# Performance work log

Hardware: AMD Instinct MI355X
Metric: run time of the kernel (lower is better)

The kernel has to match this reference:

```python
import jax, jax.numpy as jnp
import numpy as np
from jax import lax

B, H0, W0 = 8, 64, 64
DIM, HEADS, WS, SR = 128, 4, 3, 8
HD = DIM // HEADS
LOCAL = WS * WS
L_TAB = 1024
HIDDEN = int(2 * int(DIM * 4.0) / 3)  # ConvolutionalGLU hidden = 341


def _ln(x, g, b):
    m = jnp.mean(x, -1, keepdims=True)
    v = jnp.mean((x - m) ** 2, -1, keepdims=True)
    return (x - m) * lax.rsqrt(v + 1e-5) * g + b


def _l2(x):
    n = jnp.sqrt(jnp.sum(x * x, -1, keepdims=True))
    return x / jnp.maximum(n, 1e-12)


def _forward(x, norm1_g, norm1_b, q_w, kv_w, temperature, query_embedding,
             rel_bias_local, learnable_tokens, learnable_bias, sr_w, sr_b,
             normp_g, normp_b, cpb1_w, cpb1_b, cpb2_w, cpb2_b, proj_w, proj_b,
             norm2_g, norm2_b, fc1_w, fc1_b, dw_w, dw_b, fc2_w, fc2_b,
             relative_coords_table, seq_length_scale,
             relative_pos_index, padding_mask, H, W):
    Bn, N, C = x.shape
    pH, pW = H // SR, W // SR
    PL = pH * pW
    h = _ln(x, norm1_g, norm1_b)
    # ---- AggregatedAttention ----
    q = (h @ q_w.T).reshape(Bn, N, HEADS, HD).transpose(0, 2, 1, 3)  # bhnd
    q_norm = _l2(q)
    q_s = (q_norm + query_embedding) * jax.nn.softplus(temperature) * seq_length_scale
    kv = h @ kv_w.T  # (B, N, 2C)
    k_loc = _l2(kv[..., :C].reshape(Bn, N, HEADS, HD)).reshape(Bn, N, C)
    kv_loc = jnp.concatenate([k_loc, kv[..., C:]], -1).transpose(0, 2, 1).reshape(Bn, 2 * C, H, W)
    p = WS // 2
    xp = jnp.pad(kv_loc, ((0, 0), (0, 0), (p, p), (p, p)))
    # nn.Unfold(ws, pad=ws//2, stride=1): channel-major patches -> (B, 2C, LOCAL, N)
    pat = jnp.stack([xp[:, :, i:i + H, j:j + W] for i in range(WS) for j in range(WS)], axis=2)
    pat = pat.reshape(Bn, 2 * HEADS, HD, LOCAL, N).transpose(0, 1, 4, 2, 3)  # b 2h n d l
    k_l, v_l = pat[:, :HEADS], pat[:, HEADS:]
    attn_local = jnp.einsum('bhnd,bhndl->bhnl', q_s, k_l) + rel_bias_local[:, None, :]
    attn_local = jnp.where(padding_mask, -jnp.inf, attn_local)
    # pooled (global) branch
    xi = h.transpose(0, 2, 1).reshape(Bn, C, H, W)
    xi = jax.nn.gelu(jnp.einsum('oc,bchw->bohw', sr_w, xi) + sr_b[None, :, None, None], approximate=False)
    xi = xi.reshape(Bn, C, pH, SR, pW, SR).mean(axis=(3, 5)).reshape(Bn, C, PL).transpose(0, 2, 1)
    xi = _ln(xi, normp_g, normp_b)
    kvp = (xi @ kv_w.T).reshape(Bn, PL, 2 * HEADS, HD).transpose(0, 2, 1, 3)
    k_p, v_p = kvp[:, :HEADS], kvp[:, HEADS:]
    # CPB MLP bias; runtime size == trained size so both bilinear interps are identity
    t = jax.nn.relu(relative_coords_table @ cpb1_w.T + cpb1_b) @ cpb2_w.T + cpb2_b  # (L, heads)
    pb = t.T[:, relative_pos_index.reshape(-1)].reshape(HEADS, N, PL)
    attn_pool = jnp.einsum('bhnd,bhpd->bhnp', q_s, _l2(k_p)) + pb[None]
    attn = jax.nn.softmax(jnp.concatenate([attn_local, attn_pool], -1), axis=-1)
    a_l, a_p = attn[..., :LOCAL], attn[..., LOCAL:]
    l_mix = jnp.einsum('bhnd,hdl->bhnl', q_norm, learnable_tokens) + learnable_bias + a_l
    x_l = jnp.einsum('bhnl,bhndl->bhnd', l_mix, v_l)
    x_p = jnp.einsum('bhnp,bhpd->bhnd', a_p, v_p)
    attn_out = (x_l + x_p).transpose(0, 2, 1, 3).reshape(Bn, N, C) @ proj_w.T + proj_b
    x = x + attn_out
    # ---- ConvolutionalGLU MLP ----
    h2 = _ln(x, norm2_g, norm2_b)
    u = h2 @ fc1_w.T + fc1_b
    g1, v1 = u[..., :HIDDEN], u[..., HIDDEN:]
    gi = g1.transpose(0, 2, 1).reshape(Bn, HIDDEN, H, W)
    gi = lax.conv_general_dilated(gi, dw_w, (1, 1), 'SAME',
                                  feature_group_count=HIDDEN,
                                  dimension_numbers=('NCHW', 'OIHW', 'NCHW')) + dw_b[None, :, None, None]
    gi = gi.reshape(Bn, HIDDEN, N).transpose(0, 2, 1)
    mlp = (jax.nn.gelu(gi, approximate=False) * v1) @ fc2_w.T + fc2_b
    return x + mlp


def setup_inputs():
    key = jax.random.key(0)
    ks = jax.random.split(key, 16)
    N = H0 * W0
    PL = (H0 // SR) * (W0 // SR)
    r = lambda i, shape, s=0.02: jax.random.normal(ks[i], shape, jnp.float32) * s
    return {
        'x': jax.random.normal(ks[0], (B, N, DIM), jnp.float32),
        'norm1_g': jnp.ones((DIM,)), 'norm1_b': jnp.zeros((DIM,)),
        'q_w': r(1, (DIM, DIM)), 'kv_w': r(2, (2 * DIM, DIM)),
        'temperature': jnp.full((HEADS, 1, 1), float(np.log(np.expm1(1.0 / 0.24))), jnp.float32),
        'query_embedding': r(3, (HEADS, 1, HD)),
        'rel_bias_local': r(4, (HEADS, LOCAL), 0.0004),
        'learnable_tokens': r(5, (HEADS, HD, LOCAL)),
        'learnable_bias': jnp.zeros((HEADS, 1, LOCAL)),
        'sr_w': r(6, (DIM, DIM)), 'sr_b': jnp.zeros((DIM,)),
        'normp_g': jnp.ones((DIM,)), 'normp_b': jnp.zeros((DIM,)),
        'cpb1_w': r(7, (512, 2)), 'cpb1_b': jnp.zeros((512,)),
        'cpb2_w': r(8, (HEADS, 512)), 'cpb2_b': jnp.zeros((HEADS,)),
        'proj_w': r(9, (DIM, DIM)), 'proj_b': jnp.zeros((DIM,)),
        'norm2_g': jnp.ones((DIM,)), 'norm2_b': jnp.zeros((DIM,)),
        'fc1_w': r(10, (2 * HIDDEN, DIM)), 'fc1_b': jnp.zeros((2 * HIDDEN,)),
        'dw_w': r(11, (HIDDEN, 1, 3, 3)), 'dw_b': jnp.zeros((HIDDEN,)),
        'fc2_w': r(12, (DIM, HIDDEN)), 'fc2_b': jnp.zeros((DIM,)),
        'relative_coords_table': jax.random.uniform(ks[13], (L_TAB, 2), jnp.float32, -1.0, 1.0),
        'seq_length_scale': jnp.array([float(np.log(N + PL))], jnp.float32),
        'relative_pos_index': jax.random.randint(ks[14], (N, PL), 0, L_TAB),
        'padding_mask': jnp.zeros((B, 1, N, LOCAL), bool),
        'H': H0, 'W': W0,
    }


def reference(x, norm1_g, norm1_b, q_w, kv_w, temperature, query_embedding,
              rel_bias_local, learnable_tokens, learnable_bias, sr_w, sr_b,
              normp_g, normp_b, cpb1_w, cpb1_b, cpb2_w, cpb2_b, proj_w, proj_b,
              norm2_g, norm2_b, fc1_w, fc1_b, dw_w, dw_b, fc2_w, fc2_b,
              relative_coords_table, seq_length_scale,
              relative_pos_index, padding_mask, H, W):
    return _forward(x, norm1_g, norm1_b, q_w, kv_w, temperature, query_embedding,
                    rel_bias_local, learnable_tokens, learnable_bias, sr_w, sr_b,
                    normp_g, normp_b, cpb1_w, cpb1_b, cpb2_w, cpb2_b, proj_w, proj_b,
                    norm2_g, norm2_b, fc1_w, fc1_b, dw_w, dw_b, fc2_w, fc2_b,
                    relative_coords_table, seq_length_scale,
                    relative_pos_index, padding_mask, H, W)
```

## Files before the change

kernel.cpp:

```cpp
#include <hip/hip_runtime.h>
#include <hip/hip_bf16.h>
#include <math.h>

#define NTOK 4096
#define CDIM 128

typedef __attribute__((ext_vector_type(4))) float f32x4;
typedef __attribute__((ext_vector_type(8))) short bfx8;

__device__ __forceinline__ float geluf(float z){
  return 0.5f*z*(1.0f+erff(z*0.70710678118654752440f));
}
__device__ __forceinline__ float softplusf(float x){
  return (x>20.0f)?x:log1pf(expf(x));
}
__device__ __forceinline__ ushort f2bf(float f){
  __hip_bfloat16 h=__float2bfloat16(f);
  return *reinterpret_cast<ushort*>(&h);
}

__global__ __launch_bounds__(256) void convw_kernel(
  const float* __restrict__ projw, const float* __restrict__ fc1w,
  const float* __restrict__ fc2w,
  ushort* __restrict__ pwb, ushort* __restrict__ f1wb, ushort* __restrict__ f2wb){
  int id=blockIdx.x*256+threadIdx.x;
  if(id<16384) pwb[id]=f2bf(projw[id]);
  else if(id<106496){ int t=id-16384; int nn=t>>7,k=t&127;
    f1wb[t]=f2bf(nn<682? fc1w[nn*128+k] : 0.0f); }
  else if(id<155648){ int t=id-106496; int nn=t/384,k=t-nn*384;
    f2wb[t]=f2bf(k<341? fc2w[nn*341+k] : 0.0f); }
}

__global__ __launch_bounds__(128) void ln_f32_kernel(const float* __restrict__ in,
    const float* __restrict__ g, const float* __restrict__ bb, float* __restrict__ out){
  int t=blockIdx.x, c=threadIdx.x;
  float v=in[(size_t)t*CDIM+c];
  __shared__ float red[2];
  float s=v;
  #pragma unroll
  for(int m=1;m<64;m<<=1) s+=__shfl_xor(s,m);
  if((c&63)==0) red[c>>6]=s;
  __syncthreads();
  float mean=(red[0]+red[1])*(1.0f/CDIM);
  float d=v-mean;
  __syncthreads();
  float s2=d*d;
  #pragma unroll
  for(int m=1;m<64;m<<=1) s2+=__shfl_xor(s2,m);
  if((c&63)==0) red[c>>6]=s2;
  __syncthreads();
  float var=(red[0]+red[1])*(1.0f/CDIM);
  out[(size_t)t*CDIM+c]=d*rsqrtf(var+1e-5f)*g[c]+bb[c];
}

__global__ __launch_bounds__(128) void ln_bf_kernel(const float* __restrict__ in,
    const float* __restrict__ g, const float* __restrict__ bb, ushort* __restrict__ out){
  int t=blockIdx.x, c=threadIdx.x;
  float v=in[(size_t)t*CDIM+c];
  __shared__ float red[2];
  float s=v;
  #pragma unroll
  for(int m=1;m<64;m<<=1) s+=__shfl_xor(s,m);
  if((c&63)==0) red[c>>6]=s;
  __syncthreads();
  float mean=(red[0]+red[1])*(1.0f/CDIM);
  float d=v-mean;
  __syncthreads();
  float s2=d*d;
  #pragma unroll
  for(int m=1;m<64;m<<=1) s2+=__shfl_xor(s2,m);
  if((c&63)==0) red[c>>6]=s2;
  __syncthreads();
  float var=(red[0]+red[1])*(1.0f/CDIM);
  out[(size_t)t*CDIM+c]=f2bf(d*rsqrtf(var+1e-5f)*g[c]+bb[c]);
}

__global__ __launch_bounds__(128) void qproj_kernel(const float* __restrict__ h,
  const float* __restrict__ qw, const float* __restrict__ qemb,
  const float* __restrict__ temp, const float* __restrict__ seqs,
  float* __restrict__ qsout, float* __restrict__ qnout){
  int t0=blockIdx.x*8;
  int o=threadIdx.x;
  __shared__ float hr[8][128];
  for(int i=o;i<1024;i+=128) hr[i>>7][i&127]=h[(size_t)t0*128+i];
  __syncthreads();
  const float* wr=qw+(size_t)o*128;
  float a[8]={0,0,0,0,0,0,0,0};
  for(int c=0;c<128;c++){
    float wv=wr[c];
    #pragma unroll
    for(int tt=0;tt<8;tt++) a[tt]+=hr[tt][c]*wv;
  }
  int hh=o>>5, d=o&31;
  float emb=qemb[hh*32+d];
  float scale=softplusf(temp[hh])*seqs[0];
  #pragma unroll
  for(int tt=0;tt<8;tt++){
    float ss=a[tt]*a[tt];
    #pragma unroll
    for(int m=1;m<32;m<<=1) ss+=__shfl_xor(ss,m);
    float qnv=a[tt]/fmaxf(sqrtf(ss),1e-12f);
    qnout[(size_t)(t0+tt)*128+o]=qnv;
    qsout[(size_t)(t0+tt)*128+o]=(qnv+emb)*scale;
  }
}

__global__ __launch_bounds__(256) void kvproj_kernel(const float* __restrict__ h,
  const float* __restrict__ kvw, float* __restrict__ kv_tm){
  int t0=blockIdx.x*8;
  int tid=threadIdx.x;
  __shared__ float hr[8][128];
  for(int i=tid;i<1024;i+=256) hr[i>>7][i&127]=h[(size_t)t0*128+i];
  __syncthreads();
  const float* wr=kvw+(size_t)tid*128;
  float a[8]={0,0,0,0,0,0,0,0};
  for(int c=0;c<128;c++){
    float wv=wr[c];
    #pragma unroll
    for(int tt=0;tt<8;tt++) a[tt]+=hr[tt][c]*wv;
  }
  #pragma unroll
  for(int tt=0;tt<8;tt++){
    float v=a[tt];
    if(tid<128){
      float ss=v*v;
      #pragma unroll
      for(int m=1;m<32;m<<=1) ss+=__shfl_xor(ss,m);
      v/=fmaxf(sqrtf(ss),1e-12f);
    }
    kv_tm[(size_t)(t0+tt)*256+tid]=v;
  }
}

__global__ __launch_bounds__(128) void srpool_kernel(const float* __restrict__ h,
  const float* __restrict__ srw, const float* __restrict__ srb, float* __restrict__ xipre){
  int bp=blockIdx.x;
  int b=bp>>6, pp=bp&63;
  int py=pp>>3, px=pp&7;
  int o=threadIdx.x;
  __shared__ float hr[64][128];
  for(int i=0;i<64;i++){
    int yy=py*8+(i>>3), xx=px*8+(i&7);
    hr[i][o]=h[((size_t)b*NTOK+yy*64+xx)*128+o];
  }
  __syncthreads();
  const float* wr=srw+(size_t)o*128;
  float bias=srb[o];
  float acc=0;
  for(int i=0;i<64;i++){
    float s=bias;
    for(int c=0;c<128;c++) s+=hr[i][c]*wr[c];
    acc+=geluf(s);
  }
  xipre[(size_t)bp*128+o]=acc*(1.0f/64.0f);
}

__global__ __launch_bounds__(256) void kvp_kernel(const float* __restrict__ xi,
  const float* __restrict__ kvw, float* __restrict__ kpb, float* __restrict__ vpb){
  int bp=blockIdx.x;
  int b=bp>>6, p=bp&63;
  int o=threadIdx.x;
  __shared__ float xr[128];
  if(o<128) xr[o]=xi[(size_t)bp*128+o];
  __syncthreads();
  const float* wr=kvw+(size_t)o*128;
  float acc=0;
  for(int c=0;c<128;c++) acc+=xr[c]*wr[c];
  int hh=(o>>5)&3, d=o&31;
  if(o<128){
    float ss=acc*acc;
    #pragma unroll
    for(int m=1;m<32;m<<=1) ss+=__shfl_xor(ss,m);
    acc/=fmaxf(sqrtf(ss),1e-12f);
    kpb[(((size_t)b*4+hh)*64+p)*32+d]=acc;
  } else {
    vpb[(((size_t)b*4+hh)*64+p)*32+d]=acc;
  }
}

__global__ __launch_bounds__(256) void cpb_kernel(const float* __restrict__ tbl,
  const float* __restrict__ w1, const float* __restrict__ b1,
  const float* __restrict__ w2, const float* __restrict__ b2, float* __restrict__ tout){
  int i=blockIdx.x;
  float c0=tbl[i*2], c1=tbl[i*2+1];
  int tid=threadIdx.x;
  float p0=0,p1=0,p2=0,p3=0;
  for(int j=tid;j<512;j+=256){
    float r=fmaxf(c0*w1[j*2]+c1*w1[j*2+1]+b1[j],0.0f);
    p0+=r*w2[j]; p1+=r*w2[512+j]; p2+=r*w2[1024+j]; p3+=r*w2[1536+j];
  }
  #pragma unroll
  for(int m=1;m<64;m<<=1){
    p0+=__shfl_xor(p0,m); p1+=__shfl_xor(p1,m);
    p2+=__shfl_xor(p2,m); p3+=__shfl_xor(p3,m);
  }
  __shared__ float red[4][4];
  int w=tid>>6;
  if((tid&63)==0){ red[w][0]=p0; red[w][1]=p1; red[w][2]=p2; red[w][3]=p3; }
  __syncthreads();
  if(tid<4)
    tout[(size_t)i*4+tid]=red[0][tid]+red[1][tid]+red[2][tid]+red[3][tid]+b2[tid];
}

__global__ __launch_bounds__(256) void attn3b_kernel(
  const float* __restrict__ qs, const float* __restrict__ qn,
  const float* __restrict__ kv_tm, const float* __restrict__ kp,
  const float* __restrict__ vp, const float* __restrict__ tb,
  const int* __restrict__ rpi, const float* __restrict__ relb,
  const float* __restrict__ ltok, const float* __restrict__ lbias,
  ushort* __restrict__ mid){
  int n0=blockIdx.x*4, h=blockIdx.y, b=blockIdx.z;
  int tt=threadIdx.x>>6, lane=threadIdx.x&63;
  int n=n0+tt;
  int y=n>>6, x=n&63;
  __shared__ float kp_s[64][33];
  __shared__ float vp_s[64][33];
  __shared__ float qs_s[4][32], qn_s[4][32];
  __shared__ float ap_sh[4][64];
  __shared__ float lm_sh[4][9];
  {
    size_t kb=((size_t)(b*4+h))*2048;
    for(int i=threadIdx.x;i<2048;i+=256){
      kp_s[i>>5][i&31]=kp[kb+i];
      vp_s[i>>5][i&31]=vp[kb+i];
    }
  }
  if(lane<32) qs_s[tt][lane]=qs[((size_t)b*NTOK+n)*128+h*32+lane];
  else        qn_s[tt][lane-32]=qn[((size_t)b*NTOK+n)*128+h*32+(lane-32)];
  __syncthreads();
  float lp;
  {
    float s=0;
    #pragma unroll
    for(int d=0;d<32;d++) s+=qs_s[tt][d]*kp_s[lane][d];
    lp=s+tb[(size_t)rpi[(size_t)n*64+lane]*4+h];
  }
  bool lval=lane<9;
  float ll=0.0f;
  if(lval){
    int dy=lane/3-1, dx=lane%3-1;
    int yy=y+dy, xx=x+dx;
    float s=0;
    if(yy>=0&&yy<64&&xx>=0&&xx<64){
      const float* kr=kv_tm+((size_t)b*NTOK+(size_t)(yy*64+xx))*256+h*32;
      #pragma unroll
      for(int d=0;d<32;d++) s+=qs_s[tt][d]*kr[d];
    }
    ll=s+relb[h*9+lane];
  }
  float m=lp; if(lval) m=fmaxf(m,ll);
  #pragma unroll
  for(int o=1;o<64;o<<=1) m=fmaxf(m,__shfl_xor(m,o));
  float ep=expf(lp-m);
  float el=lval?expf(ll-m):0.0f;
  float ssum=ep+el;
  #pragma unroll
  for(int o=1;o<64;o<<=1) ssum+=__shfl_xor(ssum,o);
  float inv=1.0f/ssum;
  ap_sh[tt][lane]=ep*inv;
  if(lval){
    float lm=lbias[h*9+lane]+el*inv;
    #pragma unroll
    for(int d=0;d<32;d++) lm+=qn_s[tt][d]*ltok[(size_t)(h*32+d)*9+lane];
    lm_sh[tt][lane]=lm;
  }
  __syncthreads();
  if(lane<32){
    int d=lane;
    float acc=0;
    #pragma unroll
    for(int l=0;l<9;l++){
      int dy=l/3-1, dx=l%3-1;
      int yy=y+dy, xx=x+dx;
      if(yy>=0&&yy<64&&xx>=0&&xx<64)
        acc+=lm_sh[tt][l]*kv_tm[((size_t)b*NTOK+(size_t)(yy*64+xx))*256+128+h*32+d];
    }
    #pragma unroll
    for(int p=0;p<64;p++) acc+=ap_sh[tt][p]*vp_s[p][d];
    mid[((size_t)b*NTOK+n)*128+h*32+d]=f2bf(acc);
  }
}

template<int KTILES,int EPI>
__global__ __launch_bounds__(256) void gemm_kernel(
  const ushort* __restrict__ A, const ushort* __restrict__ W,
  const float* __restrict__ bias, const float* __restrict__ resid,
  float* __restrict__ out, int Nreal){
  const int Kt=KTILES*128;
  int m0=blockIdx.x*128, n0=blockIdx.y*64;
  int tid=threadIdx.x;
  int wave=tid>>6, lane=tid&63;
  __shared__ ushort lA[128*128];
  __shared__ ushort lB[64*128];
  f32x4 acc[4][2]={};
  int wm=(wave>>1)*64, wn=(wave&1)*32;
  for(int kc=0;kc<KTILES;kc++){
    __syncthreads();
    #pragma unroll
    for(int it=0;it<8;it++){
      int id=it*256+tid;
      int kb=id&15, m=id>>4;
      uint4 v=*(const uint4*)(A+(size_t)(m0+m)*Kt+kc*128+kb*8);
      int byte=(m*256+kb*16)^((m&7)<<4);
      *(uint4*)((char*)lA+byte)=v;
    }
    #pragma unroll
    for(int it=0;it<4;it++){
      int id=it*256+tid;
      int kb=id&15, n=id>>4;
      uint4 v=*(const uint4*)(W+(size_t)(n0+n)*Kt+kc*128+kb*8);
      int byte=(n*256+kb*16)^((n&7)<<4);
      *(uint4*)((char*)lB+byte)=v;
    }
    __syncthreads();
    #pragma unroll
    for(int ks=0;ks<4;ks++){
      int kb=ks*4+(lane>>4);
      bfx8 bfr[2];
      #pragma unroll
      for(int nr=0;nr<2;nr++){
        int n=wn+nr*16+(lane&15);
        int byte=(n*256+kb*16)^((n&7)<<4);
        bfr[nr]=*(bfx8*)((char*)lB+byte);
      }
      #pragma unroll
      for(int mr=0;mr<4;mr++){
        int m=wm+mr*16+(lane&15);
        int byte=(m*256+kb*16)^((m&7)<<4);
        bfx8 afr=*(bfx8*)((char*)lA+byte);
        acc[mr][0]=__builtin_amdgcn_mfma_f32_16x16x32_bf16(afr,bfr[0],acc[mr][0],0,0,0);
        acc[mr][1]=__builtin_amdgcn_mfma_f32_16x16x32_bf16(afr,bfr[1],acc[mr][1],0,0,0);
      }
    }
  }
  int g=lane>>4, li=lane&15;
  #pragma unroll
  for(int mr=0;mr<4;mr++){
    #pragma unroll
    for(int r=0;r<4;r++){
      int row=m0+wm+mr*16+g*4+r;
      #pragma unroll
      for(int nr=0;nr<2;nr++){
        int col=n0+wn+nr*16+li;
        float v=acc[mr][nr][r];
        if constexpr(EPI==0){
          if(col<Nreal) out[(size_t)row*682+col]=v+bias[col];
        } else {
          out[(size_t)row*128+col]=v+bias[col]+resid[(size_t)row*128+col];
        }
      }
    }
  }
}

__global__ __launch_bounds__(256) void dwconv_kernel(const float* __restrict__ u,
    const float* __restrict__ dww, const float* __restrict__ dwb, ushort* __restrict__ act){
  int c0=blockIdx.x*32;
  int cwReal=341-c0; if(cwReal>32) cwReal=32;
  int y0=blockIdx.y*2;
  int b=blockIdx.z;
  int tid=threadIdx.x;
  __shared__ float gsh[4][64][33];
  for(int it=0;it<32;it++){
    int idx=it*256+tid;
    int cc=idx&31;
    int px=(idx>>5)&63;
    int row=idx>>11;
    int yy=y0-1+row;
    float v=0.0f;
    if(yy>=0&&yy<64&&cc<cwReal)
      v=u[((size_t)b*NTOK+yy*64+px)*682+c0+cc];
    gsh[row][px][cc]=v;
  }
  __syncthreads();
  int cc=tid&31, pxb=tid>>5;
  int c=c0+cc;
  if(c>=384) return;
  if(cc<cwReal){
    float w0=dww[c*9+0],w1=dww[c*9+1],w2=dww[c*9+2],
          w3=dww[c*9+3],w4=dww[c*9+4],w5=dww[c*9+5],
          w6=dww[c*9+6],w7=dww[c*9+7],w8=dww[c*9+8];
    float bias=dwb[c];
    for(int ty=0;ty<2;ty++){
      for(int pxi=0;pxi<8;pxi++){
        int px=pxi*8+pxb;
        float ss=0.0f;
        if(px>0){ ss+=gsh[ty][px-1][cc]*w0+gsh[ty+1][px-1][cc]*w3+gsh[ty+2][px-1][cc]*w6; }
        ss+=gsh[ty][px][cc]*w1+gsh[ty+1][px][cc]*w4+gsh[ty+2][px][cc]*w7;
        if(px<63){ ss+=gsh[ty][px+1][cc]*w2+gsh[ty+1][px+1][cc]*w5+gsh[ty+2][px+1][cc]*w8; }
        float z=ss+bias;
        int nn=(y0+ty)*64+px;
        float gate=u[((size_t)b*NTOK+nn)*682+341+c];
        act[((size_t)b*NTOK+nn)*384+c]=f2bf(geluf(z)*gate);
      }
    }
  } else {
    for(int ty=0;ty<2;ty++)
      for(int pxi=0;pxi<8;pxi++){
        int px=pxi*8+pxb;
        int nn=(y0+ty)*64+px;
        act[((size_t)b*NTOK+nn)*384+c]=0;
      }
  }
}

extern "C" void kernel_launch(void* const* d_in, const int* in_sizes, int n_in,
                              void* d_out, int out_size, void* d_ws, size_t ws_size,
                              hipStream_t stream){
  const float* x     =(const float*)d_in[0];
  const float* n1g   =(const float*)d_in[1];
  const float* n1b   =(const float*)d_in[2];
  const float* qw    =(const float*)d_in[3];
  const float* kvw   =(const float*)d_in[4];
  const float* temp  =(const float*)d_in[5];
  const float* qemb  =(const float*)d_in[6];
  const float* relb  =(const float*)d_in[7];
  const float* ltok  =(const float*)d_in[8];
  const float* lbias =(const float*)d_in[9];
  const float* srw   =(const float*)d_in[10];
  const float* srb   =(const float*)d_in[11];
  const float* npg   =(const float*)d_in[12];
  const float* npb   =(const float*)d_in[13];
  const float* cpb1w =(const float*)d_in[14];
  const float* cpb1b =(const float*)d_in[15];
  const float* cpb2w =(const float*)d_in[16];
  const float* cpb2b =(const float*)d_in[17];
  const float* projw =(const float*)d_in[18];
  const float* projb =(const float*)d_in[19];
  const float* n2g   =(const float*)d_in[20];
  const float* n2b   =(const float*)d_in[21];
  const float* fc1w  =(const float*)d_in[22];
  const float* fc1b  =(const float*)d_in[23];
  const float* dww   =(const float*)d_in[24];
  const float* dwb   =(const float*)d_in[25];
  const float* fc2w  =(const float*)d_in[26];
  const float* fc2b  =(const float*)d_in[27];
  const float* ctab  =(const float*)d_in[28];
  const float* seqs  =(const float*)d_in[29];
  const int*   rpi   =(const int*)d_in[30];

  char* base=(char*)d_ws;
  float*  h_f32 =(float*)(base+0);
  float*  qs_b  =(float*)(base+16777216);
  float*  qn_b  =(float*)(base+33554432);
  float*  kv_tm =(float*)(base+50331648);
  ushort* mid_bf=(ushort*)(base+83886080);
  float*  x2    =(float*)(base+92274688);
  ushort* h2_bf =(ushort*)(base+109051904);
  float*  u_buf =(float*)(base+0);
  ushort* act_bf=(ushort*)(base+109051904);
  float*  xipre =(float*)(base+142606336);
  float*  xi    =(float*)(base+142868480);
  float*  kp    =(float*)(base+143130624);
  float*  vp    =(float*)(base+143392768);
  float*  tbuf  =(float*)(base+143654912);
  ushort* pwb   =(ushort*)(base+143671296);
  ushort* f1wb  =(ushort*)(base+143704064);
  ushort* f2wb  =(ushort*)(base+143884288);

  convw_kernel<<<608,256,0,stream>>>(projw,fc1w,fc2w,pwb,f1wb,f2wb);
  ln_f32_kernel<<<32768,128,0,stream>>>(x,n1g,n1b,h_f32);
  qproj_kernel<<<4096,128,0,stream>>>(h_f32,qw,qemb,temp,seqs,qs_b,qn_b);
  kvproj_kernel<<<4096,256,0,stream>>>(h_f32,kvw,kv_tm);
  srpool_kernel<<<512,128,0,stream>>>(h_f32,srw,srb,xipre);
  ln_f32_kernel<<<512,128,0,stream>>>(xipre,npg,npb,xi);
  kvp_kernel<<<512,256,0,stream>>>(xi,kvw,kp,vp);
  cpb_kernel<<<1024,256,0,stream>>>(ctab,cpb1w,cpb1b,cpb2w,cpb2b,tbuf);
  attn3b_kernel<<<dim3(1024,4,8),256,0,stream>>>(qs_b,qn_b,kv_tm,kp,vp,tbuf,rpi,relb,ltok,lbias,mid_bf);
  gemm_kernel<1,1><<<dim3(256,2),256,0,stream>>>(mid_bf,pwb,projb,x,x2,128);
  ln_bf_kernel<<<32768,128,0,stream>>>(x2,n2g,n2b,h2_bf);
  gemm_kernel<1,0><<<dim3(256,11),256,0,stream>>>(h2_bf,f1wb,fc1b,nullptr,u_buf,682);
  dwconv_kernel<<<dim3(12,32,8),256,0,stream>>>(u_buf,dww,dwb,act_bf);
  gemm_kernel<3,1><<<dim3(256,2),256,0,stream>>>(act_bf,f2wb,fc2b,x2,(float*)d_out,128);
}
```

Before: 685.6 us.

## Move q, kv and sr projections onto bf16 MFMA GEMM with fused epilogues

Replaces the scalar fp32 q-projection, kv-projection and sr-conv+pool kernels with the shared bf16 MFMA GEMM kernel. New epilogues fuse the per-head L2 normalization, query scaling and GELU, and a separate pool kernel averages the GELU output. The first LayerNorm now writes bf16, and the extra weights are converted in convw. This trades fp32 precision in these projections for matrix-core throughput, and adds an intermediate fp32 buffer for the sr output before pooling.

```diff
diff --git a/kernel.cpp b/kernel.cpp
--- a/kernel.cpp
+++ b/kernel.cpp
@@ -20,14 +20,20 @@
 }
 
 __global__ __launch_bounds__(256) void convw_kernel(
-  const float* __restrict__ projw, const float* __restrict__ fc1w,
-  const float* __restrict__ fc2w,
-  ushort* __restrict__ pwb, ushort* __restrict__ f1wb, ushort* __restrict__ f2wb){
+  const float* __restrict__ qw, const float* __restrict__ kvw,
+  const float* __restrict__ srw, const float* __restrict__ projw,
+  const float* __restrict__ fc1w, const float* __restrict__ fc2w,
+  ushort* __restrict__ qwb, ushort* __restrict__ kvwb,
+  ushort* __restrict__ srwb, ushort* __restrict__ pwb,
+  ushort* __restrict__ f1wb, ushort* __restrict__ f2wb){
   int id=blockIdx.x*256+threadIdx.x;
-  if(id<16384) pwb[id]=f2bf(projw[id]);
-  else if(id<106496){ int t=id-16384; int nn=t>>7,k=t&127;
+  if(id<16384) qwb[id]=f2bf(qw[id]);
+  else if(id<49152){ int t=id-16384; kvwb[t]=f2bf(kvw[t]); }
+  else if(id<65536){ int t=id-49152; srwb[t]=f2bf(srw[t]); }
+  else if(id<81920){ int t=id-65536; pwb[t]=f2bf(projw[t]); }
+  else if(id<172032){ int t=id-81920; int nn=t>>7,k=t&127;
     f1wb[t]=f2bf(nn<682? fc1w[nn*128+k] : 0.0f); }
-  else if(id<155648){ int t=id-106496; int nn=t/384,k=t-nn*384;
+  else if(id<221184){ int t=id-172032; int nn=t/384,k=t-nn*384;
     f2wb[t]=f2bf(k<341? fc2w[nn*341+k] : 0.0f); }
 }
 
@@ -75,84 +81,110 @@
   out[(size_t)t*CDIM+c]=f2bf(d*rsqrtf(var+1e-5f)*g[c]+bb[c]);
 }
 
-__global__ __launch_bounds__(128) void qproj_kernel(const float* __restrict__ h,
-  const float* __restrict__ qw, const float* __restrict__ qemb,
-  const float* __restrict__ temp, const float* __restrict__ seqs,
-  float* __restrict__ qsout, float* __restrict__ qnout){
-  int t0=blockIdx.x*8;
+template<int KTILES,int EPI>
+__global__ __launch_bounds__(256) void gemm_kernel(
+  const ushort* __restrict__ A, const ushort* __restrict__ W,
+  const float* __restrict__ bias, const float* __restrict__ resid,
+  float* __restrict__ out, float* __restrict__ out2, int Nreal,
+  const float* __restrict__ qemb, const float* __restrict__ temp,
+  const float* __restrict__ seqs){
+  const int Kt=KTILES*128;
+  int m0=blockIdx.x*128, n0=blockIdx.y*64;
+  int tid=threadIdx.x;
+  int wave=tid>>6, lane=tid&63;
+  __shared__ ushort lA[128*128];
+  __shared__ ushort lB[64*128];
+  f32x4 acc[4][2]={};
+  int wm=(wave>>1)*64, wn=(wave&1)*32;
+  for(int kc=0;kc<KTILES;kc++){
+    __syncthreads();
+    #pragma unroll
+    for(int it=0;it<8;it++){
+      int id=it*256+tid;
+      int kb=id&15, m=id>>4;
+      uint4 v=*(const uint4*)(A+(size_t)(m0+m)*Kt+kc*128+kb*8);
+      int byte=(m*256+kb*16)^((m&7)<<4);
+      *(uint4*)((char*)lA+byte)=v;
+    }
+    #pragma unroll
+    for(int it=0;it<4;it++){
+      int id=it*256+tid;
+      int kb=id&15, n=id>>4;
+      uint4 v=*(const uint4*)(W+(size_t)(n0+n)*Kt+kc*128+kb*8);
+      int byte=(n*256+kb*16)^((n&7)<<4);
+      *(uint4*)((char*)lB+byte)=v;
+    }
+    __syncthreads();
+    #pragma unroll
+    for(int ks=0;ks<4;ks++){
+      int kb=ks*4+(lane>>4);
+      bfx8 bfr[2];
+      #pragma unroll
+      for(int nr=0;nr<2;nr++){
+        int n=wn+nr*16+(lane&15);
+        int byte=(n*256+kb*16)^((n&7)<<4);
+        bfr[nr]=*(bfx8*)((char*)lB+byte);
+      }
+      #pragma unroll
+      for(int mr=0;mr<4;mr++){
+        int m=wm+mr*16+(lane&15);
+        int byte=(m*256+kb*16)^((m&7)<<4);
+        bfx8 afr=*(bfx8*)((char*)lA+byte);
+        acc[mr][0]=__builtin_amdgcn_mfma_f32_16x16x32_bf16(afr,bfr[0],acc[mr][0],0,0,0);
+        acc[mr][1]=__builtin_amdgcn_mfma_f32_16x16x32_bf16(afr,bfr[1],acc[mr][1],0,0,0);
+      }
+    }
+  }
+  int g=lane>>4, li=lane&15;
+  #pragma unroll
+  for(int mr=0;mr<4;mr++){
+    #pragma unroll
+    for(int r=0;r<4;r++){
+      int row=m0+wm+mr*16+g*4+r;
+      float inv=1.0f;
+      if constexpr(EPI==3||EPI==4){
+        if(EPI==3||(n0+wn)<128){
+          float s=acc[mr][0][r]*acc[mr][0][r]+acc[mr][1][r]*acc[mr][1][r];
+          s+=__shfl_xor(s,1); s+=__shfl_xor(s,2);
+          s+=__shfl_xor(s,4); s+=__shfl_xor(s,8);
+          inv=1.0f/fmaxf(sqrtf(s),1e-12f);
+        }
+      }
+      #pragma unroll
+      for(int nr=0;nr<2;nr++){
+        int col=n0+wn+nr*16+li;
+        float v=acc[mr][nr][r];
+        if constexpr(EPI==0){
+          if(col<Nreal) out[(size_t)row*682+col]=v+bias[col];
+        } else if constexpr(EPI==1){
+          out[(size_t)row*128+col]=v+bias[col]+resid[(size_t)row*128+col];
+        } else if constexpr(EPI==2){
+          out[(size_t)row*128+col]=geluf(v+bias[col]);
+        } else if constexpr(EPI==3){
+          float qn_=v*inv;
+          int head=col>>5;
+          float qs_=(qn_+qemb[col])*softplusf(temp[head])*seqs[0];
+          out[(size_t)row*128+col]=qs_;
+          out2[(size_t)row*128+col]=qn_;
+        } else {
+          float vv=((n0+wn)<128)? v*inv : v;
+          out[(size_t)row*256+col]=vv;
+        }
+      }
+    }
+  }
+}
+
+__global__ __launch_bounds__(128) void pool_kernel(const float* __restrict__ xg,
+    float* __restrict__ xp){
+  int bp=blockIdx.x; int b=bp>>6, pp=bp&63; int py=pp>>3, px=pp&7;
   int o=threadIdx.x;
-  __shared__ float hr[8][128];
-  for(int i=o;i<1024;i+=128) hr[i>>7][i&127]=h[(size_t)t0*128+i];
-  __syncthreads();
-  const float* wr=qw+(size_t)o*128;
-  float a[8]={0,0,0,0,0,0,0,0};
-  for(int c=0;c<128;c++){
-    float wv=wr[c];
-    #pragma unroll
-    for(int tt=0;tt<8;tt++) a[tt]+=hr[tt][c]*wv;
-  }
-  int hh=o>>5, d=o&31;
-  float emb=qemb[hh*32+d];
-  float scale=softplusf(temp[hh])*seqs[0];
-  #pragma unroll
-  for(int tt=0;tt<8;tt++){
-    float ss=a[tt]*a[tt];
-    #pragma unroll
-    for(int m=1;m<32;m<<=1) ss+=__shfl_xor(ss,m);
-    float qnv=a[tt]/fmaxf(sqrtf(ss),1e-12f);
-    qnout[(size_t)(t0+tt)*128+o]=qnv;
-    qsout[(size_t)(t0+tt)*128+o]=(qnv+emb)*scale;
-  }
-}
-
-__global__ __launch_bounds__(256) void kvproj_kernel(const float* __restrict__ h,
-  const float* __restrict__ kvw, float* __restrict__ kv_tm){
-  int t0=blockIdx.x*8;
-  int tid=threadIdx.x;
-  __shared__ float hr[8][128];
-  for(int i=tid;i<1024;i+=256) hr[i>>7][i&127]=h[(size_t)t0*128+i];
-  __syncthreads();
-  const float* wr=kvw+(size_t)tid*128;
-  float a[8]={0,0,0,0,0,0,0,0};
-  for(int c=0;c<128;c++){
-    float wv=wr[c];
-    #pragma unroll
-    for(int tt=0;tt<8;tt++) a[tt]+=hr[tt][c]*wv;
-  }
-  #pragma unroll
-  for(int tt=0;tt<8;tt++){
-    float v=a[tt];
-    if(tid<128){
-      float ss=v*v;
-      #pragma unroll
-      for(int m=1;m<32;m<<=1) ss+=__shfl_xor(ss,m);
-      v/=fmaxf(sqrtf(ss),1e-12f);
-    }
-    kv_tm[(size_t)(t0+tt)*256+tid]=v;
-  }
-}
-
-__global__ __launch_bounds__(128) void srpool_kernel(const float* __restrict__ h,
-  const float* __restrict__ srw, const float* __restrict__ srb, float* __restrict__ xipre){
-  int bp=blockIdx.x;
-  int b=bp>>6, pp=bp&63;
-  int py=pp>>3, px=pp&7;
-  int o=threadIdx.x;
-  __shared__ float hr[64][128];
-  for(int i=0;i<64;i++){
-    int yy=py*8+(i>>3), xx=px*8+(i&7);
-    hr[i][o]=h[((size_t)b*NTOK+yy*64+xx)*128+o];
-  }
-  __syncthreads();
-  const float* wr=srw+(size_t)o*128;
-  float bias=srb[o];
-  float acc=0;
-  for(int i=0;i<64;i++){
-    float s=bias;
-    for(int c=0;c<128;c++) s+=hr[i][c]*wr[c];
-    acc+=geluf(s);
-  }
-  xipre[(size_t)bp*128+o]=acc*(1.0f/64.0f);
+  float s=0;
+  for(int iy=0;iy<8;iy++)
+    #pragma unroll
+    for(int ix=0;ix<8;ix++)
+      s+=xg[((size_t)b*NTOK+(py*8+iy)*64+px*8+ix)*128+o];
+  xp[(size_t)bp*128+o]=s*(1.0f/64.0f);
 }
 
 __global__ __launch_bounds__(256) void kvp_kernel(const float* __restrict__ xi,
@@ -278,78 +310,6 @@
     #pragma unroll
     for(int p=0;p<64;p++) acc+=ap_sh[tt][p]*vp_s[p][d];
     mid[((size_t)b*NTOK+n)*128+h*32+d]=f2bf(acc);
-  }
-}
-
-template<int KTILES,int EPI>
-__global__ __launch_bounds__(256) void gemm_kernel(
-  const ushort* __restrict__ A, const ushort* __restrict__ W,
-  const float* __restrict__ bias, const float* __restrict__ resid,
-  float* __restrict__ out, int Nreal){
-  const int Kt=KTILES*128;
-  int m0=blockIdx.x*128, n0=blockIdx.y*64;
-  int tid=threadIdx.x;
-  int wave=tid>>6, lane=tid&63;
-  __shared__ ushort lA[128*128];
-  __shared__ ushort lB[64*128];
-  f32x4 acc[4][2]={};
-  int wm=(wave>>1)*64, wn=(wave&1)*32;
-  for(int kc=0;kc<KTILES;kc++){
-    __syncthreads();
-    #pragma unroll
-    for(int it=0;it<8;it++){
-      int id=it*256+tid;
-      int kb=id&15, m=id>>4;
-      uint4 v=*(const uint4*)(A+(size_t)(m0+m)*Kt+kc*128+kb*8);
-      int byte=(m*256+kb*16)^((m&7)<<4);
-      *(uint4*)((char*)lA+byte)=v;
-    }
-    #pragma unroll
-    for(int it=0;it<4;it++){
-      int id=it*256+tid;
-      int kb=id&15, n=id>>4;
-      uint4 v=*(const uint4*)(W+(size_t)(n0+n)*Kt+kc*128+kb*8);
-      int byte=(n*256+kb*16)^((n&7)<<4);
-      *(uint4*)((char*)lB+byte)=v;
-    }
-    __syncthreads();
-    #pragma unroll
-    for(int ks=0;ks<4;ks++){
-      int kb=ks*4+(lane>>4);
-      bfx8 bfr[2];
-      #pragma unroll
-      for(int nr=0;nr<2;nr++){
-        int n=wn+nr*16+(lane&15);
-        int byte=(n*256+kb*16)^((n&7)<<4);
-        bfr[nr]=*(bfx8*)((char*)lB+byte);
-      }
-      #pragma unroll
-      for(int mr=0;mr<4;mr++){
-        int m=wm+mr*16+(lane&15);
-        int byte=(m*256+kb*16)^((m&7)<<4);
-        bfx8 afr=*(bfx8*)((char*)lA+byte);
-        acc[mr][0]=__builtin_amdgcn_mfma_f32_16x16x32_bf16(afr,bfr[0],acc[mr][0],0,0,0);
-        acc[mr][1]=__builtin_amdgcn_mfma_f32_16x16x32_bf16(afr,bfr[1],acc[mr][1],0,0,0);
-      }
-    }
-  }
-  int g=lane>>4, li=lane&15;
-  #pragma unroll
-  for(int mr=0;mr<4;mr++){
-    #pragma unroll
-    for(int r=0;r<4;r++){
-      int row=m0+wm+mr*16+g*4+r;
-      #pragma unroll
-      for(int nr=0;nr<2;nr++){
-        int col=n0+wn+nr*16+li;
-        float v=acc[mr][nr][r];
-        if constexpr(EPI==0){
-          if(col<Nreal) out[(size_t)row*682+col]=v+bias[col];
-        } else {
-          out[(size_t)row*128+col]=v+bias[col]+resid[(size_t)row*128+col];
-        }
-      }
-    }
   }
 }
 
@@ -440,36 +400,41 @@
   const int*   rpi   =(const int*)d_in[30];
 
   char* base=(char*)d_ws;
-  float*  h_f32 =(float*)(base+0);
-  float*  qs_b  =(float*)(base+16777216);
-  float*  qn_b  =(float*)(base+33554432);
-  float*  kv_tm =(float*)(base+50331648);
-  ushort* mid_bf=(ushort*)(base+83886080);
-  float*  x2    =(float*)(base+92274688);
-  ushort* h2_bf =(ushort*)(base+109051904);
-  float*  u_buf =(float*)(base+0);
-  ushort* act_bf=(ushort*)(base+109051904);
+  ushort* h_bf  =(ushort*)(base+0);
+  float*  qs_b  =(float*)(base+8388608);
+  float*  qn_b  =(float*)(base+25165824);
+  float*  kv_tm =(float*)(base+41943040);
+  float*  xg    =(float*)(base+75497472);
+  ushort* mid_bf=(ushort*)(base+92274688);
+  float*  x2    =(float*)(base+100663296);
+  float*  u_buf =(float*)(base+8388608);
+  ushort* act_bf=(ushort*)(base+117440512);
   float*  xipre =(float*)(base+142606336);
   float*  xi    =(float*)(base+142868480);
   float*  kp    =(float*)(base+143130624);
   float*  vp    =(float*)(base+143392768);
   float*  tbuf  =(float*)(base+143654912);
-  ushort* pwb   =(ushort*)(base+143671296);
-  ushort* f1wb  =(ushort*)(base+143704064);
-  ushort* f2wb  =(ushort*)(base+143884288);
-
-  convw_kernel<<<608,256,0,stream>>>(projw,fc1w,fc2w,pwb,f1wb,f2wb);
-  ln_f32_kernel<<<32768,128,0,stream>>>(x,n1g,n1b,h_f32);
-  qproj_kernel<<<4096,128,0,stream>>>(h_f32,qw,qemb,temp,seqs,qs_b,qn_b);
-  kvproj_kernel<<<4096,256,0,stream>>>(h_f32,kvw,kv_tm);
-  srpool_kernel<<<512,128,0,stream>>>(h_f32,srw,srb,xipre);
+  ushort* qwb   =(ushort*)(base+143671296);
+  ushort* kvwb  =(ushort*)(base+143704064);
+  ushort* srwb  =(ushort*)(base+143769600);
+  ushort* pwb   =(ushort*)(base+143802368);
+  ushort* f1wb  =(ushort*)(base+143835136);
+  ushort* f2wb  =(ushort*)(base+144015360);
+  ushort* h2_bf =h_bf;
+
+  convw_kernel<<<864,256,0,stream>>>(qw,kvw,srw,projw,fc1w,fc2w,qwb,kvwb,srwb,pwb,f1wb,f2wb);
+  ln_bf_kernel<<<32768,128,0,stream>>>(x,n1g,n1b,h_bf);
+  gemm_kernel<1,3><<<dim3(256,2),256,0,stream>>>(h_bf,qwb,nullptr,nullptr,qs_b,qn_b,128,qemb,temp,seqs);
+  gemm_kernel<1,4><<<dim3(256,4),256,0,stream>>>(h_bf,kvwb,nullptr,nullptr,kv_tm,nullptr,256,nullptr,nullptr,nullptr);
+  gemm_kernel<1,2><<<dim3(256,2),256,0,stream>>>(h_bf,srwb,srb,nullptr,xg,nullptr,128,nullptr,nullptr,nullptr);
+  pool_kernel<<<512,128,0,stream>>>(xg,xipre);
   ln_f32_kernel<<<512,128,0,stream>>>(xipre,npg,npb,xi);
   kvp_kernel<<<512,256,0,stream>>>(xi,kvw,kp,vp);
   cpb_kernel<<<1024,256,0,stream>>>(ctab,cpb1w,cpb1b,cpb2w,cpb2b,tbuf);
   attn3b_kernel<<<dim3(1024,4,8),256,0,stream>>>(qs_b,qn_b,kv_tm,kp,vp,tbuf,rpi,relb,ltok,lbias,mid_bf);
-  gemm_kernel<1,1><<<dim3(256,2),256,0,stream>>>(mid_bf,pwb,projb,x,x2,128);
+  gemm_kernel<1,1><<<dim3(256,2),256,0,stream>>>(mid_bf,pwb,projb,x,x2,nullptr,128,nullptr,nullptr,nullptr);
   ln_bf_kernel<<<32768,128,0,stream>>>(x2,n2g,n2b,h2_bf);
-  gemm_kernel<1,0><<<dim3(256,11),256,0,stream>>>(h2_bf,f1wb,fc1b,nullptr,u_buf,682);
+  gemm_kernel<1,0><<<dim3(256,11),256,0,stream>>>(h2_bf,f1wb,fc1b,nullptr,u_buf,nullptr,682,nullptr,nullptr,nullptr);
   dwconv_kernel<<<dim3(12,32,8),256,0,stream>>>(u_buf,dww,dwb,act_bf);
-  gemm_kernel<3,1><<<dim3(256,2),256,0,stream>>>(act_bf,f2wb,fc2b,x2,(float*)d_out,128);
-}
+  gemm_kernel<3,1><<<dim3(256,2),256,0,stream>>>(act_bf,f2wb,fc2b,x2,(float*)d_out,nullptr,128,nullptr,nullptr,nullptr);
+}
```

After: 579.8 us. 15.4% less time.
